# Kernel optimization log

Hardware: AMD Instinct MI355X
Metric: run time of the kernel (lower is better)

The kernel has to match this reference:

```python
import jax, jax.numpy as jnp
import numpy as np

HEAD_SIZE = 128
B, L = 4, 4096

def setup_inputs() -> dict:
    key = jax.random.key(0)
    k1, k2, k3 = jax.random.split(key, 3)
    return {
        "key": jax.random.normal(k1, (B, L, HEAD_SIZE), dtype=jnp.float32),
        "query": jax.random.normal(k2, (B, L, HEAD_SIZE), dtype=jnp.float32),
        "value": jax.random.normal(k3, (B, L, HEAD_SIZE), dtype=jnp.float32),
    }

def reference(key, query, value):
    # attention scores: [B, L, L]
    scale = 1.0 / jnp.sqrt(jnp.asarray(HEAD_SIZE, dtype=query.dtype))
    att = jnp.einsum("bqd,bkd->bqk", query, key) * scale
    # causal mask (tril): positions k > q get -inf
    causal = jnp.tril(jnp.ones((att.shape[1], att.shape[2]), dtype=bool))
    att = jnp.where(causal[None, :, :], att, jnp.array(-jnp.inf, dtype=att.dtype))
    logits = jax.nn.softmax(att, axis=-1)
    # dropout omitted (eval mode / deterministic reference)
    out = jnp.einsum("bqk,bkd->bqd", logits, value)
    return out
```

## Files before the change

### kernel.cpp

```cpp
#include <hip/hip_runtime.h>

#define BB 4
#define LL 4096
#define DD 128

typedef __attribute__((ext_vector_type(8))) short short8;
typedef __attribute__((ext_vector_type(4))) float f32x4;

typedef __attribute__((address_space(1))) const unsigned int gas_u32;
typedef __attribute__((address_space(3))) unsigned int las_u32;

__device__ __forceinline__ void gload_lds16(const void* g, void* l) {
  __builtin_amdgcn_global_load_lds((gas_u32*)g, (las_u32*)l, 16, 0, 0);
}

__device__ __forceinline__ unsigned short f2bf(float x) {
  union { float f; unsigned int u; } c; c.f = x;
  unsigned int r = (c.u + 0x7FFFu + ((c.u >> 16) & 1u)) >> 16;
  return (unsigned short)r;
}
__device__ __forceinline__ float bf2f(unsigned short h) {
  union { unsigned int u; float f; } c; c.u = (unsigned int)h << 16;
  return c.f;
}

__host__ __device__ __forceinline__ int slotBase(int p) {
  int g2 = (p - 4) >> 2, w2 = (p - 4) & 3;
  return 2 * g2 * g2 + 6 * g2 + w2 * (g2 + 2);
}

__global__ __launch_bounds__(256) void prep(const float* __restrict__ K,
                                            const float* __restrict__ V,
                                            unsigned short* __restrict__ Kb,
                                            unsigned short* __restrict__ Vt) {
  __shared__ unsigned short tile[64 * 130];
  int b  = blockIdx.x >> 6;
  int kt = (blockIdx.x & 63) << 6;
  int t = threadIdx.x;
  {
    int key = t >> 2, part = t & 3;
    const float* src = K + ((size_t)b * LL + kt + key) * DD + part * 32;
    unsigned short* dst = Kb + ((size_t)b * LL + kt + key) * DD + part * 32;
#pragma unroll
    for (int j = 0; j < 4; ++j) {
      float4 x = *(const float4*)(src + j * 8);
      float4 y = *(const float4*)(src + j * 8 + 4);
      union { unsigned short h[8]; uint4 v; } o;
      o.h[0] = f2bf(x.x); o.h[1] = f2bf(x.y); o.h[2] = f2bf(x.z); o.h[3] = f2bf(x.w);
      o.h[4] = f2bf(y.x); o.h[5] = f2bf(y.y); o.h[6] = f2bf(y.z); o.h[7] = f2bf(y.w);
      *(uint4*)(dst + j * 8) = o.v;
    }
  }
  int keyi = t >> 5, dim = (t & 31) * 4;
#pragma unroll
  for (int j = 0; j < 8; ++j) {
    int key = keyi + j * 8;
    float4 x = *(const float4*)(V + ((size_t)b * LL + kt + key) * DD + dim);
    uint2 pk;
    pk.x = f2bf(x.x) | ((unsigned int)f2bf(x.y) << 16);
    pk.y = f2bf(x.z) | ((unsigned int)f2bf(x.w) << 16);
    *(uint2*)(tile + key * 130 + dim) = pk;
  }
  __syncthreads();
  int kg = (t & 7) * 8, d0 = t >> 3;
#pragma unroll
  for (int j = 0; j < 4; ++j) {
    int d = d0 + j * 32;
    union { unsigned short h[8]; uint4 v; } o;
#pragma unroll
    for (int i = 0; i < 8; ++i) o.h[i] = tile[(kg + i) * 130 + d];
    *(uint4*)(Vt + ((size_t)b * DD + d) * LL + kt + kg) = o.v;
  }
}

__global__ __launch_bounds__(256, 3) void attn_fwd(const float* __restrict__ Q,
                                                   const unsigned short* __restrict__ Kb,
                                                   const unsigned short* __restrict__ Vt,
                                                   float* __restrict__ Out,
                                                   unsigned short* __restrict__ partO,
                                                   float* __restrict__ stats,
                                                   int split) {
  __shared__ unsigned short Ks[2][32 * 128];
  __shared__ unsigned short Vs[2][128 * 32];
  __shared__ unsigned short Ps[4][32 * 40];

  int tid = threadIdx.x;
  int wave = tid >> 6;
  int lane = tid & 63;
  int l = lane & 15, gq = lane >> 4;
  int lx = l & 7;
  int vsw = (gq ^ ((l >> 1) & 3)) << 3;

  int rem = (int)blockIdx.x, p = 31, nch;
  while (true) {
    nch = split ? ((2 * p + 2 + 7) >> 3) : 1;
    int n = 4 * nch;
    if (rem < n) break;
    rem -= n; --p;
  }
  int b = rem / nch, c = rem % nch;
  int T32 = 4 * p + 4;
  int nIters = split ? min(16, T32 - c * 16) : T32;
  int ktBase = c << 9;
  int q0w = (p << 7) + wave * 32;
  int wkend = q0w + 31;
  int slot = (split && nch > 1) ? (b * 140 + slotBase(p) + c) : 0;

  const float SC = 0.08838834764831845f * 1.4426950408889634f;
  short8 qf[2][4];
#pragma unroll
  for (int mt = 0; mt < 2; ++mt) {
    const float* qp = Q + ((size_t)b * LL + q0w + mt * 16 + l) * DD + gq * 8;
#pragma unroll
    for (int cc = 0; cc < 4; ++cc) {
      float4 x = *(const float4*)(qp + cc * 32);
      float4 y = *(const float4*)(qp + cc * 32 + 4);
      short8 f;
      f[0] = (short)f2bf(x.x * SC); f[1] = (short)f2bf(x.y * SC);
      f[2] = (short)f2bf(x.z * SC); f[3] = (short)f2bf(x.w * SC);
      f[4] = (short)f2bf(y.x * SC); f[5] = (short)f2bf(y.y * SC);
      f[6] = (short)f2bf(y.z * SC); f[7] = (short)f2bf(y.w * SC);
      qf[mt][cc] = f;
    }
  }

  f32x4 acc[2][8];
#pragma unroll
  for (int mt = 0; mt < 2; ++mt)
#pragma unroll
    for (int i = 0; i < 8; ++i) acc[mt][i] = (f32x4){0.f, 0.f, 0.f, 0.f};
  f32x4 den[2];
  den[0] = (f32x4){0.f, 0.f, 0.f, 0.f};
  den[1] = (f32x4){0.f, 0.f, 0.f, 0.f};

  short8 ones;
#pragma unroll
  for (int j = 0; j < 8; ++j) ones[j] = (short)0x3F80;

  unsigned short* Pw = Ps[wave];
  const unsigned short* kgbase = Kb + (size_t)b * LL * DD;
  const unsigned short* vgbase = Vt + (size_t)b * DD * LL;

  auto stage = [&](int kt, int nb) {
#pragma unroll
    for (int j = 0; j < 2; ++j) {
      int pk_ = j * 256 + tid;
      int krow = pk_ >> 4;
      int kcol = (pk_ & 15) ^ (krow & 7);
      gload_lds16(kgbase + (size_t)(kt + krow) * DD + kcol * 8, &Ks[nb][pk_ * 8]);
      int vrow = pk_ >> 2;
      int vcol = (pk_ & 3) ^ ((vrow >> 1) & 3);
      gload_lds16(vgbase + (size_t)vrow * LL + kt + vcol * 8, &Vs[nb][pk_ * 8]);
    }
  };

  stage(ktBase, 0);
  __syncthreads();

  int cur = 0;
  for (int it = 0; it < nIters; ++it) {
    int kt = ktBase + it * 32;

    if (it + 1 < nIters) stage(kt + 32, cur ^ 1);

    if (kt <= wkend) {
      bool diag = (kt + 31 > q0w);
      const unsigned short* kbp = Ks[cur];
      const unsigned short* vbp = Vs[cur];

#pragma unroll
      for (int nt = 0; nt < 2; ++nt) {
        const unsigned short* kp = kbp + (nt * 16 + l) * 128;
        f32x4 a0 = (f32x4){0.f, 0.f, 0.f, 0.f};
        f32x4 a1 = (f32x4){0.f, 0.f, 0.f, 0.f};
#pragma unroll
        for (int cc = 0; cc < 4; ++cc) {
          short8 kf = *(const short8*)(kp + (((gq + 4 * cc) ^ lx) << 3));
          a0 = __builtin_amdgcn_mfma_f32_16x16x32_bf16(qf[0][cc], kf, a0, 0, 0, 0);
          a1 = __builtin_amdgcn_mfma_f32_16x16x32_bf16(qf[1][cc], kf, a1, 0, 0, 0);
        }
        if (diag) {
          int key = kt + nt * 16 + l;
          int qr0 = q0w + gq * 4, qr1 = q0w + 16 + gq * 4;
#pragma unroll
          for (int r = 0; r < 4; ++r) {
            if (key > qr0 + r) a0[r] = -1e30f;
            if (key > qr1 + r) a1[r] = -1e30f;
          }
        }
#pragma unroll
        for (int r = 0; r < 4; ++r) {
          Pw[(gq * 4 + r) * 40 + nt * 16 + l] = f2bf(exp2f(a0[r]));
          Pw[(16 + gq * 4 + r) * 40 + nt * 16 + l] = f2bf(exp2f(a1[r]));
        }
      }

      short8 pa0 = *(const short8*)(Pw + l * 40 + gq * 8);
      short8 pa1 = *(const short8*)(Pw + (16 + l) * 40 + gq * 8);
      den[0] = __builtin_amdgcn_mfma_f32_16x16x32_bf16(pa0, ones, den[0], 0, 0, 0);
      den[1] = __builtin_amdgcn_mfma_f32_16x16x32_bf16(pa1, ones, den[1], 0, 0, 0);
#pragma unroll
      for (int dt = 0; dt < 8; ++dt) {
        short8 vv = *(const short8*)(vbp + (dt * 16 + l) * 32 + vsw);
        acc[0][dt] = __builtin_amdgcn_mfma_f32_16x16x32_bf16(pa0, vv, acc[0][dt], 0, 0, 0);
        acc[1][dt] = __builtin_amdgcn_mfma_f32_16x16x32_bf16(pa1, vv, acc[1][dt], 0, 0, 0);
      }
    }

    __syncthreads();
    cur ^= 1;
  }

  if (!split || nch == 1) {
    float* op = Out + ((size_t)b * LL + q0w) * DD;
#pragma unroll
    for (int mt = 0; mt < 2; ++mt) {
      float inv[4];
#pragma unroll
      for (int r = 0; r < 4; ++r) inv[r] = 1.0f / den[mt][r];
#pragma unroll
      for (int dt = 0; dt < 8; ++dt)
#pragma unroll
        for (int r = 0; r < 4; ++r)
          op[(size_t)(mt * 16 + gq * 4 + r) * DD + dt * 16 + l] = acc[mt][dt][r] * inv[r];
    }
  } else {
    unsigned short* pp = partO + (size_t)slot * 16384;
#pragma unroll
    for (int mt = 0; mt < 2; ++mt) {
      int rb = wave * 32 + mt * 16;
#pragma unroll
      for (int dt = 0; dt < 8; ++dt)
#pragma unroll
        for (int r = 0; r < 4; ++r)
          pp[(rb + gq * 4 + r) * 128 + dt * 16 + l] = f2bf(acc[mt][dt][r]);
      if (l == 0) {
#pragma unroll
        for (int r = 0; r < 4; ++r)
          stats[(size_t)slot * 128 + rb + gq * 4 + r] = den[mt][r];
      }
    }
  }
}

__global__ __launch_bounds__(256) void merge(const unsigned short* __restrict__ partO,
                                             const float* __restrict__ stats,
                                             float* __restrict__ Out) {
  int b = blockIdx.x / 112;
  int rest = blockIdx.x % 112;
  int p = 4 + rest / 4;
  int rg = rest % 4;
  int nch = (2 * p + 2 + 7) >> 3;
  int slot0 = b * 140 + slotBase(p);

  int tid = threadIdx.x;
  int row = rg * 32 + (tid >> 3);
  int dcol = (tid & 7) * 16;

  float lsum = 0.f;
  for (int cc = 0; cc < nch; ++cc)
    lsum += stats[(size_t)(slot0 + cc) * 128 + row];
  float inv = 1.0f / lsum;

  float o[16];
#pragma unroll
  for (int j = 0; j < 16; ++j) o[j] = 0.f;
  for (int cc = 0; cc < nch; ++cc) {
    const unsigned short* pp = partO + (size_t)(slot0 + cc) * 16384 + (size_t)row * 128 + dcol;
#pragma unroll
    for (int j = 0; j < 16; ++j) o[j] += bf2f(pp[j]);
  }
  float* op = Out + ((size_t)b * LL + (p << 7) + row) * DD + dcol;
#pragma unroll
  for (int j = 0; j < 4; ++j) {
    float4 v; v.x = o[j*4] * inv; v.y = o[j*4+1] * inv; v.z = o[j*4+2] * inv; v.w = o[j*4+3] * inv;
    *(float4*)(op + j * 4) = v;
  }
}

extern "C" void kernel_launch(void* const* d_in, const int* in_sizes, int n_in,
                              void* d_out, int out_size, void* d_ws, size_t ws_size,
                              hipStream_t stream) {
  const float* K = (const float*)d_in[0];
  const float* Q = (const float*)d_in[1];
  const float* V = (const float*)d_in[2];
  float* Out = (float*)d_out;

  const size_t convBytes = (size_t)2 * BB * LL * DD * 2;
  unsigned short* Kb = (unsigned short*)d_ws;
  unsigned short* Vt = Kb + (size_t)BB * LL * DD;

  size_t slots = (size_t)BB * 140;
  size_t need = convBytes + slots * 16384 * 2 + slots * 128 * 4;
  int split = (ws_size >= need) ? 1 : 0;

  unsigned short* partO = (unsigned short*)((char*)d_ws + convBytes);
  float* stats = (float*)((char*)d_ws + convBytes + slots * 16384 * 2);

  int nBlocks = 0;
  for (int p = 0; p < 32; ++p) nBlocks += 4 * (split ? ((2 * p + 2 + 7) >> 3) : 1);

  prep<<<dim3(BB * (LL / 64)), dim3(256), 0, stream>>>(K, V, Kb, Vt);
  attn_fwd<<<dim3(nBlocks), dim3(256), 0, stream>>>(Q, Kb, Vt, Out, partO, stats, split);
  if (split)
    merge<<<dim3(BB * 112), dim3(256), 0, stream>>>(partO, stats, Out);
}
```

Baseline: 122.8 us.

## Make causal KV split size configurable, raise occupancy, swizzle P tile in LDS

The fixed 16-tile KV chunking of the split-K causal attention becomes a runtime chunk size. When the workspace is large enough it uses 8-tile chunks, which launches more, shorter blocks for better load balance across CUs. Slot indexing is generalized with a prefix count, and the merge kernel is adapted to match. The launch-bounds occupancy hint goes from 3 to 4 blocks per CU, and the padded P scratch tile (stride 40) becomes an unpadded stride-32 XOR-swizzled layout to cut LDS use and bank conflicts. The trade-offs are more partial-output traffic and merge work, and possible register spills under the tighter register budget.

```diff
diff --git a/kernel.cpp b/kernel.cpp
--- a/kernel.cpp
+++ b/kernel.cpp
@@ -22,11 +22,6 @@
 __device__ __forceinline__ float bf2f(unsigned short h) {
   union { unsigned int u; float f; } c; c.u = (unsigned int)h << 16;
   return c.f;
-}
-
-__host__ __device__ __forceinline__ int slotBase(int p) {
-  int g2 = (p - 4) >> 2, w2 = (p - 4) & 3;
-  return 2 * g2 * g2 + 6 * g2 + w2 * (g2 + 2);
 }
 
 __global__ __launch_bounds__(256) void prep(const float* __restrict__ K,
@@ -73,16 +68,16 @@
   }
 }
 
-__global__ __launch_bounds__(256, 3) void attn_fwd(const float* __restrict__ Q,
+__global__ __launch_bounds__(256, 4) void attn_fwd(const float* __restrict__ Q,
                                                    const unsigned short* __restrict__ Kb,
                                                    const unsigned short* __restrict__ Vt,
                                                    float* __restrict__ Out,
                                                    unsigned short* __restrict__ partO,
                                                    float* __restrict__ stats,
-                                                   int split) {
+                                                   int split, int ch, int totch) {
   __shared__ unsigned short Ks[2][32 * 128];
   __shared__ unsigned short Vs[2][128 * 32];
-  __shared__ unsigned short Ps[4][32 * 40];
+  __shared__ unsigned short Ps[4][32 * 32];
 
   int tid = threadIdx.x;
   int wave = tid >> 6;
@@ -90,21 +85,23 @@
   int l = lane & 15, gq = lane >> 4;
   int lx = l & 7;
   int vsw = (gq ^ ((l >> 1) & 3)) << 3;
-
-  int rem = (int)blockIdx.x, p = 31, nch;
+  int prc = ((gq ^ (l >> 2)) & 3) << 3;
+
+  int rem = (int)blockIdx.x, p = 31, nch, acc = totch;
   while (true) {
-    nch = split ? ((2 * p + 2 + 7) >> 3) : 1;
+    nch = split ? ((4 * p + 4 + ch - 1) / ch) : 1;
+    acc -= nch;
     int n = 4 * nch;
     if (rem < n) break;
     rem -= n; --p;
   }
   int b = rem / nch, c = rem % nch;
   int T32 = 4 * p + 4;
-  int nIters = split ? min(16, T32 - c * 16) : T32;
-  int ktBase = c << 9;
+  int nIters = split ? min(ch, T32 - c * ch) : T32;
+  int ktBase = c * (ch << 5);
   int q0w = (p << 7) + wave * 32;
   int wkend = q0w + 31;
-  int slot = (split && nch > 1) ? (b * 140 + slotBase(p) + c) : 0;
+  int slot = (split && nch > 1) ? (b * totch + acc + c) : 0;
 
   const float SC = 0.08838834764831845f * 1.4426950408889634f;
   short8 qf[2][4];
@@ -124,11 +121,11 @@
     }
   }
 
-  f32x4 acc[2][8];
+  f32x4 acc2[2][8];
 #pragma unroll
   for (int mt = 0; mt < 2; ++mt)
 #pragma unroll
-    for (int i = 0; i < 8; ++i) acc[mt][i] = (f32x4){0.f, 0.f, 0.f, 0.f};
+    for (int i = 0; i < 8; ++i) acc2[mt][i] = (f32x4){0.f, 0.f, 0.f, 0.f};
   f32x4 den[2];
   den[0] = (f32x4){0.f, 0.f, 0.f, 0.f};
   den[1] = (f32x4){0.f, 0.f, 0.f, 0.f};
@@ -188,22 +185,23 @@
             if (key > qr1 + r) a1[r] = -1e30f;
           }
         }
+        int pc = (l & 7) + ((((nt << 1) | (l >> 3)) ^ gq) & 3) * 8;
 #pragma unroll
         for (int r = 0; r < 4; ++r) {
-          Pw[(gq * 4 + r) * 40 + nt * 16 + l] = f2bf(exp2f(a0[r]));
-          Pw[(16 + gq * 4 + r) * 40 + nt * 16 + l] = f2bf(exp2f(a1[r]));
+          Pw[(gq * 4 + r) * 32 + pc] = f2bf(exp2f(a0[r]));
+          Pw[(16 + gq * 4 + r) * 32 + pc] = f2bf(exp2f(a1[r]));
         }
       }
 
-      short8 pa0 = *(const short8*)(Pw + l * 40 + gq * 8);
-      short8 pa1 = *(const short8*)(Pw + (16 + l) * 40 + gq * 8);
+      short8 pa0 = *(const short8*)(Pw + l * 32 + prc);
+      short8 pa1 = *(const short8*)(Pw + (16 + l) * 32 + prc);
       den[0] = __builtin_amdgcn_mfma_f32_16x16x32_bf16(pa0, ones, den[0], 0, 0, 0);
       den[1] = __builtin_amdgcn_mfma_f32_16x16x32_bf16(pa1, ones, den[1], 0, 0, 0);
 #pragma unroll
       for (int dt = 0; dt < 8; ++dt) {
         short8 vv = *(const short8*)(vbp + (dt * 16 + l) * 32 + vsw);
-        acc[0][dt] = __builtin_amdgcn_mfma_f32_16x16x32_bf16(pa0, vv, acc[0][dt], 0, 0, 0);
-        acc[1][dt] = __builtin_amdgcn_mfma_f32_16x16x32_bf16(pa1, vv, acc[1][dt], 0, 0, 0);
+        acc2[0][dt] = __builtin_amdgcn_mfma_f32_16x16x32_bf16(pa0, vv, acc2[0][dt], 0, 0, 0);
+        acc2[1][dt] = __builtin_amdgcn_mfma_f32_16x16x32_bf16(pa1, vv, acc2[1][dt], 0, 0, 0);
       }
     }
 
@@ -222,7 +220,7 @@
       for (int dt = 0; dt < 8; ++dt)
 #pragma unroll
         for (int r = 0; r < 4; ++r)
-          op[(size_t)(mt * 16 + gq * 4 + r) * DD + dt * 16 + l] = acc[mt][dt][r] * inv[r];
+          op[(size_t)(mt * 16 + gq * 4 + r) * DD + dt * 16 + l] = acc2[mt][dt][r] * inv[r];
     }
   } else {
     unsigned short* pp = partO + (size_t)slot * 16384;
@@ -233,7 +231,7 @@
       for (int dt = 0; dt < 8; ++dt)
 #pragma unroll
         for (int r = 0; r < 4; ++r)
-          pp[(rb + gq * 4 + r) * 128 + dt * 16 + l] = f2bf(acc[mt][dt][r]);
+          pp[(rb + gq * 4 + r) * 128 + dt * 16 + l] = f2bf(acc2[mt][dt][r]);
       if (l == 0) {
 #pragma unroll
         for (int r = 0; r < 4; ++r)
@@ -245,13 +243,18 @@
 
 __global__ __launch_bounds__(256) void merge(const unsigned short* __restrict__ partO,
                                              const float* __restrict__ stats,
-                                             float* __restrict__ Out) {
-  int b = blockIdx.x / 112;
-  int rest = blockIdx.x % 112;
-  int p = 4 + rest / 4;
+                                             float* __restrict__ Out,
+                                             int ch, int totch) {
+  int pMin = ch >> 2;
+  int per = (32 - pMin) * 4;
+  int b = blockIdx.x / per;
+  int rest = blockIdx.x % per;
+  int p = pMin + rest / 4;
   int rg = rest % 4;
-  int nch = (2 * p + 2 + 7) >> 3;
-  int slot0 = b * 140 + slotBase(p);
+  int nch = (4 * p + 4 + ch - 1) / ch;
+  int pre = 0;
+  for (int k = 0; k < p; ++k) pre += (4 * k + 4 + ch - 1) / ch;
+  int slot0 = b * totch + pre;
 
   int tid = threadIdx.x;
   int row = rg * 32 + (tid >> 3);
@@ -290,18 +293,30 @@
   unsigned short* Kb = (unsigned short*)d_ws;
   unsigned short* Vt = Kb + (size_t)BB * LL * DD;
 
-  size_t slots = (size_t)BB * 140;
-  size_t need = convBytes + slots * 16384 * 2 + slots * 128 * 4;
-  int split = (ws_size >= need) ? 1 : 0;
+  int t8 = 0, t16 = 0;
+  for (int p = 0; p < 32; ++p) {
+    t8  += (4 * p + 4 + 7) >> 3;
+    t16 += (4 * p + 4 + 15) >> 4;
+  }
+  size_t need8  = convBytes + (size_t)BB * t8  * (32768 + 512);
+  size_t need16 = convBytes + (size_t)BB * t16 * (32768 + 512);
+
+  int split = 0, ch = 16, totch = t16;
+  if (ws_size >= need8)       { split = 1; ch = 8;  totch = t8;  }
+  else if (ws_size >= need16) { split = 1; ch = 16; totch = t16; }
 
   unsigned short* partO = (unsigned short*)((char*)d_ws + convBytes);
-  float* stats = (float*)((char*)d_ws + convBytes + slots * 16384 * 2);
+  float* stats = (float*)((char*)d_ws + convBytes + (size_t)BB * totch * 32768);
 
   int nBlocks = 0;
-  for (int p = 0; p < 32; ++p) nBlocks += 4 * (split ? ((2 * p + 2 + 7) >> 3) : 1);
+  for (int p = 0; p < 32; ++p)
+    nBlocks += 4 * (split ? ((4 * p + 4 + ch - 1) / ch) : 1);
 
   prep<<<dim3(BB * (LL / 64)), dim3(256), 0, stream>>>(K, V, Kb, Vt);
-  attn_fwd<<<dim3(nBlocks), dim3(256), 0, stream>>>(Q, Kb, Vt, Out, partO, stats, split);
-  if (split)
-    merge<<<dim3(BB * 112), dim3(256), 0, stream>>>(partO, stats, Out);
-}
+  attn_fwd<<<dim3(nBlocks), dim3(256), 0, stream>>>(Q, Kb, Vt, Out, partO, stats,
+                                                    split, ch, totch);
+  if (split) {
+    int pMin = ch >> 2;
+    merge<<<dim3(BB * (32 - pMin) * 4), dim3(256), 0, stream>>>(partO, stats, Out, ch, totch);
+  }
+}
```

New measurement: 177.0 us. 1.44x slower.

## Load K and V tiles directly from global memory instead of LDS staging

Applied to the files above, without the earlier changes.

Removes the double-buffered LDS staging of K and V tiles via global_load_lds along with the block-wide barriers. Each wave now reads its K and V fragments straight from global memory into registers and stops iterating at its own causal end. Occupancy in launch_bounds goes from 3 to 4 blocks. The trade is losing the sharing of tiles across the 4 waves and the prefetch overlap, in exchange for no syncs, less LDS use and per-wave early exit.

```diff
diff --git a/kernel.cpp b/kernel.cpp
--- a/kernel.cpp
+++ b/kernel.cpp
@@ -6,13 +6,6 @@
 
 typedef __attribute__((ext_vector_type(8))) short short8;
 typedef __attribute__((ext_vector_type(4))) float f32x4;
-
-typedef __attribute__((address_space(1))) const unsigned int gas_u32;
-typedef __attribute__((address_space(3))) unsigned int las_u32;
-
-__device__ __forceinline__ void gload_lds16(const void* g, void* l) {
-  __builtin_amdgcn_global_load_lds((gas_u32*)g, (las_u32*)l, 16, 0, 0);
-}
 
 __device__ __forceinline__ unsigned short f2bf(float x) {
   union { float f; unsigned int u; } c; c.f = x;
@@ -73,23 +66,19 @@
   }
 }
 
-__global__ __launch_bounds__(256, 3) void attn_fwd(const float* __restrict__ Q,
+__global__ __launch_bounds__(256, 4) void attn_fwd(const float* __restrict__ Q,
                                                    const unsigned short* __restrict__ Kb,
                                                    const unsigned short* __restrict__ Vt,
                                                    float* __restrict__ Out,
                                                    unsigned short* __restrict__ partO,
                                                    float* __restrict__ stats,
                                                    int split) {
-  __shared__ unsigned short Ks[2][32 * 128];
-  __shared__ unsigned short Vs[2][128 * 32];
   __shared__ unsigned short Ps[4][32 * 40];
 
   int tid = threadIdx.x;
   int wave = tid >> 6;
   int lane = tid & 63;
   int l = lane & 15, gq = lane >> 4;
-  int lx = l & 7;
-  int vsw = (gq ^ ((l >> 1) & 3)) << 3;
 
   int rem = (int)blockIdx.x, p = 31, nch;
   while (true) {
@@ -138,77 +127,67 @@
   for (int j = 0; j < 8; ++j) ones[j] = (short)0x3F80;
 
   unsigned short* Pw = Ps[wave];
-  const unsigned short* kgbase = Kb + (size_t)b * LL * DD;
-  const unsigned short* vgbase = Vt + (size_t)b * DD * LL;
-
-  auto stage = [&](int kt, int nb) {
-#pragma unroll
-    for (int j = 0; j < 2; ++j) {
-      int pk_ = j * 256 + tid;
-      int krow = pk_ >> 4;
-      int kcol = (pk_ & 15) ^ (krow & 7);
-      gload_lds16(kgbase + (size_t)(kt + krow) * DD + kcol * 8, &Ks[nb][pk_ * 8]);
-      int vrow = pk_ >> 2;
-      int vcol = (pk_ & 3) ^ ((vrow >> 1) & 3);
-      gload_lds16(vgbase + (size_t)vrow * LL + kt + vcol * 8, &Vs[nb][pk_ * 8]);
-    }
-  };
-
-  stage(ktBase, 0);
-  __syncthreads();
-
-  int cur = 0;
-  for (int it = 0; it < nIters; ++it) {
+  const unsigned short* kg = Kb + (size_t)b * LL * DD;
+  const unsigned short* vg = Vt + (size_t)b * DD * LL;
+
+  int nEff = nIters;
+  {
+    int lt = ((wkend - ktBase) >> 5) + 1;
+    if (lt < nEff) nEff = lt;
+    if (nEff < 0) nEff = 0;
+  }
+
+  for (int it = 0; it < nEff; ++it) {
     int kt = ktBase + it * 32;
-
-    if (it + 1 < nIters) stage(kt + 32, cur ^ 1);
-
-    if (kt <= wkend) {
-      bool diag = (kt + 31 > q0w);
-      const unsigned short* kbp = Ks[cur];
-      const unsigned short* vbp = Vs[cur];
-
-#pragma unroll
-      for (int nt = 0; nt < 2; ++nt) {
-        const unsigned short* kp = kbp + (nt * 16 + l) * 128;
-        f32x4 a0 = (f32x4){0.f, 0.f, 0.f, 0.f};
-        f32x4 a1 = (f32x4){0.f, 0.f, 0.f, 0.f};
-#pragma unroll
-        for (int cc = 0; cc < 4; ++cc) {
-          short8 kf = *(const short8*)(kp + (((gq + 4 * cc) ^ lx) << 3));
-          a0 = __builtin_amdgcn_mfma_f32_16x16x32_bf16(qf[0][cc], kf, a0, 0, 0, 0);
-          a1 = __builtin_amdgcn_mfma_f32_16x16x32_bf16(qf[1][cc], kf, a1, 0, 0, 0);
-        }
-        if (diag) {
-          int key = kt + nt * 16 + l;
-          int qr0 = q0w + gq * 4, qr1 = q0w + 16 + gq * 4;
-#pragma unroll
-          for (int r = 0; r < 4; ++r) {
-            if (key > qr0 + r) a0[r] = -1e30f;
-            if (key > qr1 + r) a1[r] = -1e30f;
-          }
-        }
+    bool diag = (kt + 31 > q0w);
+
+#pragma unroll
+    for (int nt = 0; nt < 2; ++nt) {
+      const unsigned short* kp = kg + (size_t)(kt + nt * 16 + l) * DD + gq * 8;
+      short8 k0 = *(const short8*)(kp);
+      short8 k1 = *(const short8*)(kp + 32);
+      short8 k2 = *(const short8*)(kp + 64);
+      short8 k3 = *(const short8*)(kp + 96);
+      f32x4 a0 = (f32x4){0.f, 0.f, 0.f, 0.f};
+      f32x4 a1 = (f32x4){0.f, 0.f, 0.f, 0.f};
+      a0 = __builtin_amdgcn_mfma_f32_16x16x32_bf16(qf[0][0], k0, a0, 0, 0, 0);
+      a1 = __builtin_amdgcn_mfma_f32_16x16x32_bf16(qf[1][0], k0, a1, 0, 0, 0);
+      a0 = __builtin_amdgcn_mfma_f32_16x16x32_bf16(qf[0][1], k1, a0, 0, 0, 0);
+      a1 = __builtin_amdgcn_mfma_f32_16x16x32_bf16(qf[1][1], k1, a1, 0, 0, 0);
+      a0 = __builtin_amdgcn_mfma_f32_16x16x32_bf16(qf[0][2], k2, a0, 0, 0, 0);
+      a1 = __builtin_amdgcn_mfma_f32_16x16x32_bf16(qf[1][2], k2, a1, 0, 0, 0);
+      a0 = __builtin_amdgcn_mfma_f32_16x16x32_bf16(qf[0][3], k3, a0, 0, 0, 0);
+      a1 = __builtin_amdgcn_mfma_f32_16x16x32_bf16(qf[1][3], k3, a1, 0, 0, 0);
+      if (diag) {
+        int key = kt + nt * 16 + l;
+        int qr0 = q0w + gq * 4, qr1 = q0w + 16 + gq * 4;
 #pragma unroll
         for (int r = 0; r < 4; ++r) {
-          Pw[(gq * 4 + r) * 40 + nt * 16 + l] = f2bf(exp2f(a0[r]));
-          Pw[(16 + gq * 4 + r) * 40 + nt * 16 + l] = f2bf(exp2f(a1[r]));
+          if (key > qr0 + r) a0[r] = -1e30f;
+          if (key > qr1 + r) a1[r] = -1e30f;
         }
       }
-
-      short8 pa0 = *(const short8*)(Pw + l * 40 + gq * 8);
-      short8 pa1 = *(const short8*)(Pw + (16 + l) * 40 + gq * 8);
-      den[0] = __builtin_amdgcn_mfma_f32_16x16x32_bf16(pa0, ones, den[0], 0, 0, 0);
-      den[1] = __builtin_amdgcn_mfma_f32_16x16x32_bf16(pa1, ones, den[1], 0, 0, 0);
-#pragma unroll
-      for (int dt = 0; dt < 8; ++dt) {
-        short8 vv = *(const short8*)(vbp + (dt * 16 + l) * 32 + vsw);
-        acc[0][dt] = __builtin_amdgcn_mfma_f32_16x16x32_bf16(pa0, vv, acc[0][dt], 0, 0, 0);
-        acc[1][dt] = __builtin_amdgcn_mfma_f32_16x16x32_bf16(pa1, vv, acc[1][dt], 0, 0, 0);
+#pragma unroll
+      for (int r = 0; r < 4; ++r) {
+        Pw[(gq * 4 + r) * 40 + nt * 16 + l] = f2bf(exp2f(a0[r]));
+        Pw[(16 + gq * 4 + r) * 40 + nt * 16 + l] = f2bf(exp2f(a1[r]));
       }
     }
 
-    __syncthreads();
-    cur ^= 1;
+    short8 vv[8];
+#pragma unroll
+    for (int dt = 0; dt < 8; ++dt)
+      vv[dt] = *(const short8*)(vg + (size_t)(dt * 16 + l) * LL + kt + gq * 8);
+
+    short8 pa0 = *(const short8*)(Pw + l * 40 + gq * 8);
+    short8 pa1 = *(const short8*)(Pw + (16 + l) * 40 + gq * 8);
+    den[0] = __builtin_amdgcn_mfma_f32_16x16x32_bf16(pa0, ones, den[0], 0, 0, 0);
+    den[1] = __builtin_amdgcn_mfma_f32_16x16x32_bf16(pa1, ones, den[1], 0, 0, 0);
+#pragma unroll
+    for (int dt = 0; dt < 8; ++dt) {
+      acc[0][dt] = __builtin_amdgcn_mfma_f32_16x16x32_bf16(pa0, vv[dt], acc[0][dt], 0, 0, 0);
+      acc[1][dt] = __builtin_amdgcn_mfma_f32_16x16x32_bf16(pa1, vv[dt], acc[1][dt], 0, 0, 0);
+    }
   }
 
   if (!split || nch == 1) {
```

New measurement: 225.8 us. 83.9% more time.

## Shrink attention query tile to 64 rows with 16 rows per wave

Applied to the files above, without the earlier changes.

Each attention block now covers 64 query rows instead of 128, with each wave handling one 16-row MFMA tile instead of two. The smaller per-wave register footprint allows the launch bound to rise to four blocks per SM, and the finer tiles give more, smaller blocks to spread the causal workload. Split-chunk slot indexing, the partial-output size, the stats layout and the merge kernel are rewritten for the 64-row tiles. In exchange, each staged K/V tile feeds half as many MFMAs, so K/V traffic from L2 and LDS staging per unit of compute roughly doubles, and the merge kernel now recomputes its slot prefix with a loop.

```diff
diff --git a/kernel.cpp b/kernel.cpp
--- a/kernel.cpp
+++ b/kernel.cpp
@@ -22,11 +22,6 @@
 __device__ __forceinline__ float bf2f(unsigned short h) {
   union { unsigned int u; float f; } c; c.u = (unsigned int)h << 16;
   return c.f;
-}
-
-__host__ __device__ __forceinline__ int slotBase(int p) {
-  int g2 = (p - 4) >> 2, w2 = (p - 4) & 3;
-  return 2 * g2 * g2 + 6 * g2 + w2 * (g2 + 2);
 }
 
 __global__ __launch_bounds__(256) void prep(const float* __restrict__ K,
@@ -73,7 +68,7 @@
   }
 }
 
-__global__ __launch_bounds__(256, 3) void attn_fwd(const float* __restrict__ Q,
+__global__ __launch_bounds__(256, 4) void attn_fwd(const float* __restrict__ Q,
                                                    const unsigned short* __restrict__ Kb,
                                                    const unsigned short* __restrict__ Vt,
                                                    float* __restrict__ Out,
@@ -82,7 +77,7 @@
                                                    int split) {
   __shared__ unsigned short Ks[2][32 * 128];
   __shared__ unsigned short Vs[2][128 * 32];
-  __shared__ unsigned short Ps[4][32 * 40];
+  __shared__ unsigned short Ps[4][16 * 40];
 
   int tid = threadIdx.x;
   int wave = tid >> 6;
@@ -91,26 +86,26 @@
   int lx = l & 7;
   int vsw = (gq ^ ((l >> 1) & 3)) << 3;
 
-  int rem = (int)blockIdx.x, p = 31, nch;
+  int rem = (int)blockIdx.x, p = 63, nch, accq = 288;
   while (true) {
-    nch = split ? ((2 * p + 2 + 7) >> 3) : 1;
+    nch = split ? ((p + 8) >> 3) : 1;
+    accq -= nch;
     int n = 4 * nch;
     if (rem < n) break;
     rem -= n; --p;
   }
   int b = rem / nch, c = rem % nch;
-  int T32 = 4 * p + 4;
+  int T32 = 2 * (p + 1);
   int nIters = split ? min(16, T32 - c * 16) : T32;
   int ktBase = c << 9;
-  int q0w = (p << 7) + wave * 32;
-  int wkend = q0w + 31;
-  int slot = (split && nch > 1) ? (b * 140 + slotBase(p) + c) : 0;
+  int q0w = (p << 6) + wave * 16;
+  int wkend = q0w + 15;
+  int slot = (split && nch > 1) ? (b * 288 + accq + c) : 0;
 
   const float SC = 0.08838834764831845f * 1.4426950408889634f;
-  short8 qf[2][4];
-#pragma unroll
-  for (int mt = 0; mt < 2; ++mt) {
-    const float* qp = Q + ((size_t)b * LL + q0w + mt * 16 + l) * DD + gq * 8;
+  short8 qf[4];
+  {
+    const float* qp = Q + ((size_t)b * LL + q0w + l) * DD + gq * 8;
 #pragma unroll
     for (int cc = 0; cc < 4; ++cc) {
       float4 x = *(const float4*)(qp + cc * 32);
@@ -120,18 +115,14 @@
       f[2] = (short)f2bf(x.z * SC); f[3] = (short)f2bf(x.w * SC);
       f[4] = (short)f2bf(y.x * SC); f[5] = (short)f2bf(y.y * SC);
       f[6] = (short)f2bf(y.z * SC); f[7] = (short)f2bf(y.w * SC);
-      qf[mt][cc] = f;
-    }
-  }
-
-  f32x4 acc[2][8];
-#pragma unroll
-  for (int mt = 0; mt < 2; ++mt)
-#pragma unroll
-    for (int i = 0; i < 8; ++i) acc[mt][i] = (f32x4){0.f, 0.f, 0.f, 0.f};
-  f32x4 den[2];
-  den[0] = (f32x4){0.f, 0.f, 0.f, 0.f};
-  den[1] = (f32x4){0.f, 0.f, 0.f, 0.f};
+      qf[cc] = f;
+    }
+  }
+
+  f32x4 oacc[8];
+#pragma unroll
+  for (int i = 0; i < 8; ++i) oacc[i] = (f32x4){0.f, 0.f, 0.f, 0.f};
+  f32x4 den = (f32x4){0.f, 0.f, 0.f, 0.f};
 
   short8 ones;
 #pragma unroll
@@ -172,38 +163,29 @@
       for (int nt = 0; nt < 2; ++nt) {
         const unsigned short* kp = kbp + (nt * 16 + l) * 128;
         f32x4 a0 = (f32x4){0.f, 0.f, 0.f, 0.f};
-        f32x4 a1 = (f32x4){0.f, 0.f, 0.f, 0.f};
 #pragma unroll
         for (int cc = 0; cc < 4; ++cc) {
           short8 kf = *(const short8*)(kp + (((gq + 4 * cc) ^ lx) << 3));
-          a0 = __builtin_amdgcn_mfma_f32_16x16x32_bf16(qf[0][cc], kf, a0, 0, 0, 0);
-          a1 = __builtin_amdgcn_mfma_f32_16x16x32_bf16(qf[1][cc], kf, a1, 0, 0, 0);
+          a0 = __builtin_amdgcn_mfma_f32_16x16x32_bf16(qf[cc], kf, a0, 0, 0, 0);
         }
         if (diag) {
           int key = kt + nt * 16 + l;
-          int qr0 = q0w + gq * 4, qr1 = q0w + 16 + gq * 4;
-#pragma unroll
-          for (int r = 0; r < 4; ++r) {
+          int qr0 = q0w + gq * 4;
+#pragma unroll
+          for (int r = 0; r < 4; ++r)
             if (key > qr0 + r) a0[r] = -1e30f;
-            if (key > qr1 + r) a1[r] = -1e30f;
-          }
         }
 #pragma unroll
-        for (int r = 0; r < 4; ++r) {
+        for (int r = 0; r < 4; ++r)
           Pw[(gq * 4 + r) * 40 + nt * 16 + l] = f2bf(exp2f(a0[r]));
-          Pw[(16 + gq * 4 + r) * 40 + nt * 16 + l] = f2bf(exp2f(a1[r]));
-        }
       }
 
       short8 pa0 = *(const short8*)(Pw + l * 40 + gq * 8);
-      short8 pa1 = *(const short8*)(Pw + (16 + l) * 40 + gq * 8);
-      den[0] = __builtin_amdgcn_mfma_f32_16x16x32_bf16(pa0, ones, den[0], 0, 0, 0);
-      den[1] = __builtin_amdgcn_mfma_f32_16x16x32_bf16(pa1, ones, den[1], 0, 0, 0);
+      den = __builtin_amdgcn_mfma_f32_16x16x32_bf16(pa0, ones, den, 0, 0, 0);
 #pragma unroll
       for (int dt = 0; dt < 8; ++dt) {
         short8 vv = *(const short8*)(vbp + (dt * 16 + l) * 32 + vsw);
-        acc[0][dt] = __builtin_amdgcn_mfma_f32_16x16x32_bf16(pa0, vv, acc[0][dt], 0, 0, 0);
-        acc[1][dt] = __builtin_amdgcn_mfma_f32_16x16x32_bf16(pa1, vv, acc[1][dt], 0, 0, 0);
+        oacc[dt] = __builtin_amdgcn_mfma_f32_16x16x32_bf16(pa0, vv, oacc[dt], 0, 0, 0);
       }
     }
 
@@ -213,32 +195,26 @@
 
   if (!split || nch == 1) {
     float* op = Out + ((size_t)b * LL + q0w) * DD;
-#pragma unroll
-    for (int mt = 0; mt < 2; ++mt) {
-      float inv[4];
-#pragma unroll
-      for (int r = 0; r < 4; ++r) inv[r] = 1.0f / den[mt][r];
-#pragma unroll
-      for (int dt = 0; dt < 8; ++dt)
-#pragma unroll
-        for (int r = 0; r < 4; ++r)
-          op[(size_t)(mt * 16 + gq * 4 + r) * DD + dt * 16 + l] = acc[mt][dt][r] * inv[r];
-    }
+    float inv[4];
+#pragma unroll
+    for (int r = 0; r < 4; ++r) inv[r] = 1.0f / den[r];
+#pragma unroll
+    for (int dt = 0; dt < 8; ++dt)
+#pragma unroll
+      for (int r = 0; r < 4; ++r)
+        op[(size_t)(gq * 4 + r) * DD + dt * 16 + l] = oacc[dt][r] * inv[r];
   } else {
-    unsigned short* pp = partO + (size_t)slot * 16384;
-#pragma unroll
-    for (int mt = 0; mt < 2; ++mt) {
-      int rb = wave * 32 + mt * 16;
-#pragma unroll
-      for (int dt = 0; dt < 8; ++dt)
-#pragma unroll
-        for (int r = 0; r < 4; ++r)
-          pp[(rb + gq * 4 + r) * 128 + dt * 16 + l] = f2bf(acc[mt][dt][r]);
-      if (l == 0) {
-#pragma unroll
-        for (int r = 0; r < 4; ++r)
-          stats[(size_t)slot * 128 + rb + gq * 4 + r] = den[mt][r];
-      }
+    unsigned short* pp = partO + (size_t)slot * 8192;
+    int rb = wave * 16;
+#pragma unroll
+    for (int dt = 0; dt < 8; ++dt)
+#pragma unroll
+      for (int r = 0; r < 4; ++r)
+        pp[(rb + gq * 4 + r) * 128 + dt * 16 + l] = f2bf(oacc[dt][r]);
+    if (l == 0) {
+#pragma unroll
+      for (int r = 0; r < 4; ++r)
+        stats[(size_t)slot * 64 + rb + gq * 4 + r] = den[r];
     }
   }
 }
@@ -248,10 +224,12 @@
                                              float* __restrict__ Out) {
   int b = blockIdx.x / 112;
   int rest = blockIdx.x % 112;
-  int p = 4 + rest / 4;
-  int rg = rest % 4;
-  int nch = (2 * p + 2 + 7) >> 3;
-  int slot0 = b * 140 + slotBase(p);
+  int p = 8 + rest / 2;
+  int rg = rest % 2;
+  int nch = (p + 8) >> 3;
+  int pre = 0;
+  for (int k = 0; k < p; ++k) pre += (k + 8) >> 3;
+  int slot0 = b * 288 + pre;
 
   int tid = threadIdx.x;
   int row = rg * 32 + (tid >> 3);
@@ -259,18 +237,18 @@
 
   float lsum = 0.f;
   for (int cc = 0; cc < nch; ++cc)
-    lsum += stats[(size_t)(slot0 + cc) * 128 + row];
+    lsum += stats[(size_t)(slot0 + cc) * 64 + row];
   float inv = 1.0f / lsum;
 
   float o[16];
 #pragma unroll
   for (int j = 0; j < 16; ++j) o[j] = 0.f;
   for (int cc = 0; cc < nch; ++cc) {
-    const unsigned short* pp = partO + (size_t)(slot0 + cc) * 16384 + (size_t)row * 128 + dcol;
+    const unsigned short* pp = partO + (size_t)(slot0 + cc) * 8192 + (size_t)row * 128 + dcol;
 #pragma unroll
     for (int j = 0; j < 16; ++j) o[j] += bf2f(pp[j]);
   }
-  float* op = Out + ((size_t)b * LL + (p << 7) + row) * DD + dcol;
+  float* op = Out + ((size_t)b * LL + (p << 6) + row) * DD + dcol;
 #pragma unroll
   for (int j = 0; j < 4; ++j) {
     float4 v; v.x = o[j*4] * inv; v.y = o[j*4+1] * inv; v.z = o[j*4+2] * inv; v.w = o[j*4+3] * inv;
@@ -290,15 +268,16 @@
   unsigned short* Kb = (unsigned short*)d_ws;
   unsigned short* Vt = Kb + (size_t)BB * LL * DD;
 
-  size_t slots = (size_t)BB * 140;
-  size_t need = convBytes + slots * 16384 * 2 + slots * 128 * 4;
+  size_t slots = (size_t)BB * 288;
+  size_t need = convBytes + slots * 16384 + slots * 64 * 4;
   int split = (ws_size >= need) ? 1 : 0;
 
   unsigned short* partO = (unsigned short*)((char*)d_ws + convBytes);
-  float* stats = (float*)((char*)d_ws + convBytes + slots * 16384 * 2);
+  float* stats = (float*)((char*)d_ws + convBytes + slots * 16384);
 
   int nBlocks = 0;
-  for (int p = 0; p < 32; ++p) nBlocks += 4 * (split ? ((2 * p + 2 + 7) >> 3) : 1);
+  for (int p = 0; p < 64; ++p)
+    nBlocks += 4 * (split ? ((p + 8) >> 3) : 1);
 
   prep<<<dim3(BB * (LL / 64)), dim3(256), 0, stream>>>(K, V, Kb, Vt);
   attn_fwd<<<dim3(nBlocks), dim3(256), 0, stream>>>(Q, Kb, Vt, Out, partO, stats, split);
```

Measured after the change: 128.4 us. 1.05x slower.
